# Optimization experiments

Hardware: AMD Instinct MI355X
Metric: run time of the kernel (lower is better)

The kernel has to match this reference:

```python
import jax, jax.numpy as jnp
import numpy as np

L, C = 32, 32          # latent_length, latent_classes
REC = 2048             # recurrent_size
PRIOR_COEF, POST_COEF, FREE_NAT = 0.8, 0.2, 1.0


def _kl(logits_p, logits_q):
    p = jax.nn.softmax(logits_p, axis=-1)
    log_p = jax.nn.log_softmax(logits_p, axis=-1)
    log_q = jax.nn.log_softmax(logits_q, axis=-1)
    return (p * (log_p - log_q)).sum(axis=(-2, -1))


def setup_inputs() -> dict:
    key = jax.random.key(0)
    ks = jax.random.split(key, 16)
    B, T = 256, 64
    s = 0.02  # weight scale to keep activations sane
    return {
        "zs": jax.random.normal(ks[0], (B, T, 4, 16, 32), jnp.float32),
        "actions": jax.random.normal(ks[1], (B, T, 3), jnp.float32),
        "z_mean": jnp.zeros((4, 1, 1), jnp.float32),
        "z_std": jnp.ones((4, 1, 1), jnp.float32),
        "enc_W": jax.random.normal(ks[2], (2048, 1024), jnp.float32) * s,
        "enc_b": jnp.zeros((1024,), jnp.float32),
        "pre_W": jax.random.normal(ks[3], (1027, 1024), jnp.float32) * s,
        "pre_b": jnp.zeros((1024,), jnp.float32),
        "W_ih": jax.random.normal(ks[4], (3 * REC, 1024), jnp.float32) * s,
        "W_hh": jax.random.normal(ks[5], (3 * REC, REC), jnp.float32) * s,
        "b_ih": jnp.zeros((3 * REC,), jnp.float32),
        "b_hh": jnp.zeros((3 * REC,), jnp.float32),
        "tW1": jax.random.normal(ks[6], (REC, 1024), jnp.float32) * s,
        "tb1": jnp.zeros((1024,), jnp.float32),
        "tW2": jax.random.normal(ks[7], (1024, L * C), jnp.float32) * s,
        "tb2": jnp.zeros((L * C,), jnp.float32),
        "rW1": jax.random.normal(ks[8], (REC + 1024, 1024), jnp.float32) * s,
        "rb1": jnp.zeros((1024,), jnp.float32),
        "rW2": jax.random.normal(ks[9], (1024, L * C), jnp.float32) * s,
        "rb2": jnp.zeros((L * C,), jnp.float32),
        "dW1": jax.random.normal(ks[10], (REC + L * C, 1024), jnp.float32) * s,
        "db1": jnp.zeros((1024,), jnp.float32),
        "dW2": jax.random.normal(ks[11], (1024, 2048), jnp.float32) * s,
        "db2": jnp.zeros((2048,), jnp.float32),
    }


def reference(zs, actions, z_mean, z_std, enc_W, enc_b, pre_W, pre_b,
              W_ih, W_hh, b_ih, b_hh, tW1, tb1, tW2, tb2,
              rW1, rb1, rW2, rb2, dW1, db1, dW2, db2):
    B, T = zs.shape[:2]
    zs_norm = (zs - z_mean) / z_std                      # (B,T,4,16,32)
    flat = zs_norm.reshape(B, T, -1)                      # (B,T,2048)
    encoded = jax.nn.elu(flat @ enc_W + enc_b)            # (B,T,1024)

    h0 = jnp.zeros((B, REC), zs.dtype)
    lat0 = jnp.zeros((B, L * C), zs.dtype)

    def step(carry, xs):
        h, lat = carry
        a_prev, emb = xs                                  # (B,3), (B,1024)
        # recurrent model: pre-MLP + GRU cell (PyTorch GRUCell math)
        x = jax.nn.elu(jnp.concatenate([lat, a_prev], -1) @ pre_W + pre_b)
        gx = x @ W_ih.T + b_ih                            # (B,3*REC)
        gh = h @ W_hh.T + b_hh
        xr, xz, xn = jnp.split(gx, 3, axis=-1)
        hr, hz, hn = jnp.split(gh, 3, axis=-1)
        r = jax.nn.sigmoid(xr + hr)
        u = jax.nn.sigmoid(xz + hz)
        n = jnp.tanh(xn + r * hn)
        h_new = (1.0 - u) * n + u * h
        # transition (prior) logits
        prior = (jax.nn.elu(h_new @ tW1 + tb1) @ tW2 + tb2).reshape(B, L, C)
        # representation (posterior) logits + straight-through one-hot sample
        post = (jax.nn.elu(jnp.concatenate([h_new, emb], -1) @ rW1 + rb1)
                @ rW2 + rb2).reshape(B, L, C)
        probs = jax.nn.softmax(post, axis=-1)
        one_hot = jax.nn.one_hot(jnp.argmax(post, -1), C, dtype=post.dtype)
        lat_new = (one_hot + probs - jax.lax.stop_gradient(probs)).reshape(B, L * C)
        return (h_new, lat_new), (h_new, lat_new, prior, post)

    xs = (jnp.swapaxes(actions[:, :-1], 0, 1),            # (T-1,B,3)
          jnp.swapaxes(encoded[:, 1:], 0, 1))             # (T-1,B,1024)
    _, (hiddens, latents, priors, posts) = jax.lax.scan(step, (h0, lat0), xs)
    hiddens = jnp.swapaxes(hiddens, 0, 1)                 # (B,T-1,REC)
    latents = jnp.swapaxes(latents, 0, 1)                 # (B,T-1,L*C)
    priors = jnp.swapaxes(priors, 0, 1)                   # (B,T-1,L,C)
    posts = jnp.swapaxes(posts, 0, 1)

    dec_in = jnp.concatenate([hiddens, latents], -1)
    pred = (jax.nn.elu(dec_in @ dW1 + db1) @ dW2 + db2).reshape(B, T - 1, 4, 16, 32)

    recon = jnp.mean((pred - zs_norm[:, 1:]) ** 2)
    prior_loss = PRIOR_COEF * jnp.maximum(
        _kl(jax.lax.stop_gradient(posts), priors), FREE_NAT)
    post_loss = POST_COEF * jnp.maximum(
        _kl(posts, jax.lax.stop_gradient(priors)), FREE_NAT)
    kl_loss = jnp.mean(prior_loss + post_loss)
    return recon + kl_loss
```

## Files before the change

kernel.cpp:

```cpp
#include <hip/hip_runtime.h>
#include <hip/hip_bf16.h>
#include <math.h>

typedef unsigned short u16;
typedef __attribute__((ext_vector_type(8))) short s16x8;
typedef __attribute__((ext_vector_type(4))) short s16x4;
typedef __attribute__((ext_vector_type(4))) float f32x4;

#define DEVI static __device__ __forceinline__

DEVI u16 f2bfu(float f) {
    unsigned u = __float_as_uint(f);
    unsigned r = (u + 0x7fffu + ((u >> 16) & 1u)) >> 16;
    return (u16)r;
}
DEVI float bfu2f(u16 u) { return __uint_as_float(((unsigned)u) << 16); }
DEVI float eluf(float x) { return x > 0.f ? x : (expf(x) - 1.f); }
DEVI float sigm(float x) { return 1.f / (1.f + expf(-x)); }

#define GLOAD16(gsrc, ldst)                                                            \
    __builtin_amdgcn_global_load_lds(                                                  \
        (__attribute__((address_space(1))) void*)(void*)(gsrc),                        \
        (__attribute__((address_space(3))) void*)(ldst), 16, 0, 0)

template <int N> DEVI void vmwait();
template <> DEVI void vmwait<0>() { asm volatile("s_waitcnt vmcnt(0)" ::: "memory"); }
template <> DEVI void vmwait<4>() { asm volatile("s_waitcnt vmcnt(4)" ::: "memory"); }
template <> DEVI void vmwait<5>() { asm volatile("s_waitcnt vmcnt(5)" ::: "memory"); }

struct GP {
    const u16* A; int lda;
    const u16* Bt;
    float* Cf; u16* Cb; int ldc;
    const float* bias;
    const u16* aux; int auxld;
    const float* zs;
    const float* zmean; const float* zstd;
    double* accum;
    int* idx;
    int K; int gridN; int rbase;
};

template <int MF, int NF, int EPI, bool DUAL>
__global__ __launch_bounds__(256) void gemm_k(GP p0, GP p1) {
    GP p = (DUAL && blockIdx.y) ? p1 : p0;
    constexpr int BM = 32 * MF, BN = 32 * NF;
    constexpr int ABYTES = BM * 64, BBYTES = BN * 64;

    const int tid = threadIdx.x;
    const int w = tid >> 6, lane = tid & 63;
    const int bid = blockIdx.x;
    const int bn = bid % p.gridN, bm = bid / p.gridN;
    const int r0 = bm * BM, c0 = bn * BN;
    const int wm = w >> 1, wn = w & 1;

    __shared__ __attribute__((aligned(16))) char sm[2 * (ABYTES + BBYTES)];
    __shared__ float ps[4];

    auto stage = [&](int kt, int buf) {
        char* s = sm + buf * (ABYTES + BBYTES);
        const u16* Ag = p.A + (size_t)r0 * p.lda + kt * 32;
#pragma unroll
        for (int it = 0; it < BM / 64; ++it) {
            int bo = it * 4096 + w * 1024 + lane * 16;
            int row = bo >> 6, kg = (bo & 63) >> 4;
            GLOAD16(Ag + (size_t)row * p.lda + kg * 8, s + bo);
        }
        const u16* Bg = p.Bt + (size_t)c0 * p.K + kt * 32;
        char* sb = s + ABYTES;
#pragma unroll
        for (int it = 0; it < BN / 64; ++it) {
            int bo = it * 4096 + w * 1024 + lane * 16;
            int row = bo >> 6, kg = (bo & 63) >> 4;
            GLOAD16(Bg + (size_t)row * p.K + kg * 8, sb + bo);
        }
    };

    f32x4 acc[MF][NF];
#pragma unroll
    for (int mf = 0; mf < MF; ++mf)
#pragma unroll
        for (int nf = 0; nf < NF; ++nf) acc[mf][nf] = (f32x4){0.f, 0.f, 0.f, 0.f};

    const int nk = p.K >> 5;
    stage(0, 0);
    asm volatile("s_waitcnt vmcnt(0)" ::: "memory");
    __syncthreads();
    int cur = 0;
    for (int kt = 0; kt < nk; ++kt) {
        if (kt + 1 < nk) stage(kt + 1, cur ^ 1);
        const char* s = sm + cur * (ABYTES + BBYTES);
        s16x8 aF[MF], bF[NF];
#pragma unroll
        for (int mf = 0; mf < MF; ++mf)
            aF[mf] = *(const s16x8*)(s + ((wm * MF + mf) * 16 + (lane & 15)) * 64 + (lane >> 4) * 16);
#pragma unroll
        for (int nf = 0; nf < NF; ++nf)
            bF[nf] = *(const s16x8*)(s + ABYTES + ((wn * NF + nf) * 16 + (lane & 15)) * 64 + (lane >> 4) * 16);
#pragma unroll
        for (int mf = 0; mf < MF; ++mf)
#pragma unroll
            for (int nf = 0; nf < NF; ++nf)
                acc[mf][nf] = __builtin_amdgcn_mfma_f32_16x16x32_bf16(aF[mf], bF[nf], acc[mf][nf], 0, 0, 0);
        asm volatile("s_waitcnt vmcnt(0)" ::: "memory");
        __syncthreads();
        cur ^= 1;
    }

    const int lrow4 = (lane >> 4) << 2, lcol = lane & 15;
    float lsum = 0.f;
#pragma unroll
    for (int mf = 0; mf < MF; ++mf) {
        int rowb = r0 + (wm * MF + mf) * 16 + lrow4;
#pragma unroll
        for (int nf = 0; nf < NF; ++nf) {
            int col = c0 + (wn * NF + nf) * 16 + lcol;
#pragma unroll
            for (int j = 0; j < 4; ++j) {
                float v = acc[mf][nf][j];
                int r = rowb + j;
                if constexpr (EPI == 1) {
                    p.Cb[(size_t)r * p.ldc + col] = f2bfu(eluf(v + p.bias[col]));
                } else if constexpr (EPI == 2) {
                    p.Cb[(size_t)r * p.ldc + col] = f2bfu(v + p.bias[col]);
                } else if constexpr (EPI == 4) {
                    p.Cb[(size_t)r * p.ldc + col] = f2bfu(eluf(v + bfu2f(p.aux[(size_t)r * p.auxld + col])));
                } else if constexpr (EPI == 5) {
                    v += p.bias[col];
                    int R = r + p.rbase;
                    int tt = R >> 8, b = R & 255;
                    int ch = col >> 9;
                    float z = (p.zs[((size_t)b * 64 + tt + 1) * 2048 + col] - p.zmean[ch]) / p.zstd[ch];
                    float d = v - z;
                    lsum += d * d;
                }
            }
        }
    }
    if constexpr (EPI == 5) {
#pragma unroll
        for (int o = 32; o > 0; o >>= 1) lsum += __shfl_down(lsum, o, 64);
        if (lane == 0) ps[w] = lsum;
        __syncthreads();
        if (tid == 0) {
            double s = (double)ps[0] + (double)ps[1] + (double)ps[2] + (double)ps[3];
            atomicAdd(p.accum, s);
        }
    }
}

template <int EPI, int MF, int NF>
DEVI void epiS(const GP& p, f32x4 (&acc)[MF][NF], int r0, int c0, int wm, int wn,
               int lrow4, int lcol) {
#pragma unroll
    for (int mf = 0; mf < MF; ++mf) {
        int rowb = r0 + (wm * MF + mf) * 16 + lrow4;
#pragma unroll
        for (int nf = 0; nf < NF; ++nf) {
            int col = c0 + (wn * NF + nf) * 16 + lcol;
#pragma unroll
            for (int j = 0; j < 4; ++j) {
                float v = acc[mf][nf][j];
                int r = rowb + j;
                if constexpr (EPI == 4) {
                    p.Cb[(size_t)r * p.ldc + col] = f2bfu(eluf(v + bfu2f(p.aux[(size_t)r * p.auxld + col])));
                } else if constexpr (EPI == 7) {
                    p.Cb[(size_t)r * p.ldc + col] = f2bfu(v + p.bias[col]);
                }
            }
        }
    }
}

template <int WM, int WN, int MF, int NF, int EPIa, int EPIb>
__global__ __launch_bounds__(WM * WN * 64) void gemmS(GP pa, GP pb, int nA) {
    constexpr int NT = WM * WN * 64;
    constexpr int BM = WM * MF * 16, BN = WN * NF * 16;
    constexpr int ABY = BM * 128, BBY = BN * 128;
    constexpr int LPT = (ABY + BBY) / (NT * 16);

    const int tid = threadIdx.x, w = tid >> 6, lane = tid & 63;
    const bool isA = (int)blockIdx.x < nA;
    GP p = isA ? pa : pb;
    const int bid = isA ? blockIdx.x : blockIdx.x - nA;
    const int bn = bid % p.gridN, bm = bid / p.gridN;
    const int r0 = bm * BM, c0 = bn * BN;
    const int wm = w / WN, wn = w % WN;

    __shared__ __attribute__((aligned(16))) char sm[3 * (ABY + BBY)];

    auto stage = [&](int kt, int buf) {
        char* s = sm + buf * (ABY + BBY);
#pragma unroll
        for (int it = 0; it < ABY / (NT * 16); ++it) {
            int bo = it * (NT * 16) + tid * 16;
            int row = bo >> 7, kb = bo & 127;
            int kbs = kb ^ ((row & 7) << 4);
            GLOAD16(p.A + (size_t)(r0 + row) * p.lda + kt * 64 + (kbs >> 1), s + bo);
        }
        char* sb = s + ABY;
#pragma unroll
        for (int it = 0; it < BBY / (NT * 16); ++it) {
            int bo = it * (NT * 16) + tid * 16;
            int row = bo >> 7, kb = bo & 127;
            int kbs = kb ^ ((row & 7) << 4);
            GLOAD16(p.Bt + (size_t)(c0 + row) * p.K + kt * 64 + (kbs >> 1), sb + bo);
        }
    };

    f32x4 acc[MF][NF];
#pragma unroll
    for (int mf = 0; mf < MF; ++mf)
#pragma unroll
        for (int nf = 0; nf < NF; ++nf) acc[mf][nf] = (f32x4){0.f, 0.f, 0.f, 0.f};

    const int nk = p.K >> 6;
    stage(0, 0);
    stage(1, 1);
    int b0 = 0, b1 = 1, b2 = 2;
    for (int kt = 0; kt < nk; ++kt) {
        if (kt < nk - 1) vmwait<LPT>(); else vmwait<0>();
        __builtin_amdgcn_sched_barrier(0);
        __builtin_amdgcn_s_barrier();
        if (kt + 2 < nk) stage(kt + 2, b2);
        const char* s = sm + b0 * (ABY + BBY);
#pragma unroll
        for (int ks = 0; ks < 2; ++ks) {
            const int kb = ks * 64 + ((lane >> 4) << 4);
            s16x8 aF[MF], bF[NF];
#pragma unroll
            for (int mf = 0; mf < MF; ++mf) {
                int rt = (wm * MF + mf) * 16 + (lane & 15);
                aF[mf] = *(const s16x8*)(s + rt * 128 + (kb ^ ((rt & 7) << 4)));
            }
#pragma unroll
            for (int nf = 0; nf < NF; ++nf) {
                int rt = (wn * NF + nf) * 16 + (lane & 15);
                bF[nf] = *(const s16x8*)(s + ABY + rt * 128 + (kb ^ ((rt & 7) << 4)));
            }
#pragma unroll
            for (int mf = 0; mf < MF; ++mf)
#pragma unroll
                for (int nf = 0; nf < NF; ++nf)
                    acc[mf][nf] = __builtin_amdgcn_mfma_f32_16x16x32_bf16(aF[mf], bF[nf], acc[mf][nf], 0, 0, 0);
        }
        int t_ = b0; b0 = b1; b1 = b2; b2 = t_;
    }

    const int lrow4 = (lane >> 4) << 2, lcol = lane & 15;
    if constexpr (EPIa == 8) {
        const int lat = (c0 >> 5) + wn;
#pragma unroll
        for (int mf = 0; mf < MF; ++mf) {
#pragma unroll
            for (int j = 0; j < 4; ++j) {
                int r = r0 + (wm * MF + mf) * 16 + lrow4 + j;
                int col0 = c0 + wn * 32 + lcol;
                float v0 = acc[mf][0][j] + p.bias[col0];
                float v1 = acc[mf][1][j] + p.bias[col0 + 16];
                p.Cb[(size_t)r * p.ldc + col0] = f2bfu(v0);
                p.Cb[(size_t)r * p.ldc + col0 + 16] = f2bfu(v1);
                float mv; int mi;
                if (v1 > v0) { mv = v1; mi = lcol + 16; } else { mv = v0; mi = lcol; }
#pragma unroll
                for (int o = 8; o >= 1; o >>= 1) {
                    float ov = __shfl_xor(mv, o, 64);
                    int oi = __shfl_xor(mi, o, 64);
                    if (ov > mv || (ov == mv && oi < mi)) { mv = ov; mi = oi; }
                }
                if (lcol == 0) p.idx[(size_t)r * 32 + lat] = mi;
            }
        }
    } else {
        if (isA) epiS<EPIa, MF, NF>(p, acc, r0, c0, wm, wn, lrow4, lcol);
        else     epiS<EPIb, MF, NF>(p, acc, r0, c0, wm, wn, lrow4, lcol);
    }
}

template <bool FIRST>
__global__ __launch_bounds__(256) void k_gates(const u16* __restrict__ X, const u16* __restrict__ WihB,
                                               const float* __restrict__ bih, const float* __restrict__ bhh,
                                               const u16* __restrict__ GHb, float* __restrict__ hf32,
                                               u16* __restrict__ hallT) {
    constexpr int ABY = 64 * 128;
    constexpr int BTB = 32 * 128;
    constexpr int TSZ = ABY + 3 * BTB;
    const int tid = threadIdx.x, w = tid >> 6, lane = tid & 63;
    const int bm = blockIdx.x >> 6, bn = blockIdx.x & 63;
    const int r0 = bm * 64, c0 = bn * 32;
    const int wm = w >> 1, wn = w & 1;

    __shared__ __attribute__((aligned(16))) char sm[3 * TSZ];

    auto stage = [&](int kt, int buf) {
        char* s = sm + buf * TSZ;
#pragma unroll
        for (int it = 0; it < 2; ++it) {
            int bo = it * 4096 + tid * 16;
            int row = bo >> 7, kb = bo & 127;
            int kbs = kb ^ ((row & 7) << 4);
            GLOAD16(X + (size_t)(r0 + row) * 1024 + kt * 64 + (kbs >> 1), s + bo);
        }
        char* sb = s + ABY;
#pragma unroll
        for (int g = 0; g < 3; ++g) {
            int bo = tid * 16;
            int row = bo >> 7, kb = bo & 127;
            int kbs = kb ^ ((row & 7) << 4);
            GLOAD16(WihB + (size_t)(g * 2048 + c0 + row) * 1024 + kt * 64 + (kbs >> 1), sb + g * BTB + bo);
        }
    };

    f32x4 acc[3][2];
#pragma unroll
    for (int g = 0; g < 3; ++g)
#pragma unroll
        for (int mf = 0; mf < 2; ++mf) acc[g][mf] = (f32x4){0.f, 0.f, 0.f, 0.f};

    stage(0, 0);
    stage(1, 1);
    int b0 = 0, b1 = 1, b2 = 2;
    for (int kt = 0; kt < 16; ++kt) {
        if (kt < 15) vmwait<5>(); else vmwait<0>();
        __builtin_amdgcn_sched_barrier(0);
        __builtin_amdgcn_s_barrier();
        if (kt + 2 < 16) stage(kt + 2, b2);
        const char* s = sm + b0 * TSZ;
#pragma unroll
        for (int ks = 0; ks < 2; ++ks) {
            const int kb = ks * 64 + ((lane >> 4) << 4);
            s16x8 aF[2], bF[3];
#pragma unroll
            for (int mf = 0; mf < 2; ++mf) {
                int rt = (wm * 2 + mf) * 16 + (lane & 15);
                aF[mf] = *(const s16x8*)(s + rt * 128 + (kb ^ ((rt & 7) << 4)));
            }
#pragma unroll
            for (int g = 0; g < 3; ++g) {
                int rt = wn * 16 + (lane & 15);
                bF[g] = *(const s16x8*)(s + ABY + g * BTB + rt * 128 + (kb ^ ((rt & 7) << 4)));
            }
#pragma unroll
            for (int g = 0; g < 3; ++g)
#pragma unroll
                for (int mf = 0; mf < 2; ++mf)
                    acc[g][mf] = __builtin_amdgcn_mfma_f32_16x16x32_bf16(aF[mf], bF[g], acc[g][mf], 0, 0, 0);
        }
        int t_ = b0; b0 = b1; b1 = b2; b2 = t_;
    }

    const int lrow4 = (lane >> 4) << 2, lcol = lane & 15;
    const int cc = c0 + wn * 16 + lcol;
#pragma unroll
    for (int mf = 0; mf < 2; ++mf) {
        int rr0 = r0 + (wm * 2 + mf) * 16 + lrow4;
#pragma unroll
        for (int j = 0; j < 4; ++j) {
            int rr = rr0 + j;
            float xr = acc[0][mf][j] + bih[cc];
            float xz = acc[1][mf][j] + bih[2048 + cc];
            float xn = acc[2][mf][j] + bih[4096 + cc];
            float hr_, hz_, hn_;
            if (FIRST) { hr_ = bhh[cc]; hz_ = bhh[2048 + cc]; hn_ = bhh[4096 + cc]; }
            else {
                const u16* g = GHb + (size_t)rr * 6144;
                hr_ = bfu2f(g[cc]); hz_ = bfu2f(g[2048 + cc]); hn_ = bfu2f(g[4096 + cc]);
            }
            float r = sigm(xr + hr_);
            float u = sigm(xz + hz_);
            float n = tanhf(xn + r * hn_);
            float hold = FIRST ? 0.f : hf32[(size_t)rr * 2048 + cc];
            float h = (1.f - u) * n + u * hold;
            hf32[(size_t)rr * 2048 + cc] = h;
            hallT[(size_t)rr * 2048 + cc] = f2bfu(h);
        }
    }
}

__global__ void k_init(double* acc) { acc[0] = 0.0; acc[1] = 0.0; }

__global__ void k_cast(const float* __restrict__ src, u16* __restrict__ dst, int n4) {
    int i = blockIdx.x * 256 + threadIdx.x;
    if (i >= n4) return;
    f32x4 v = *(const f32x4*)(src + (size_t)i * 4);
    s16x4 o;
    o[0] = (short)f2bfu(v[0]); o[1] = (short)f2bfu(v[1]);
    o[2] = (short)f2bfu(v[2]); o[3] = (short)f2bfu(v[3]);
    *(s16x4*)(dst + (size_t)i * 4) = o;
}

__global__ void k_transpose(const float* __restrict__ src, int sld, u16* __restrict__ dst, int K) {
    __shared__ float tile[32][33];
    int k0 = blockIdx.x * 32, n0 = blockIdx.y * 32;
    for (int r = threadIdx.y; r < 32; r += 8)
        tile[r][threadIdx.x] = src[(size_t)(k0 + r) * sld + n0 + threadIdx.x];
    __syncthreads();
    for (int r = threadIdx.y; r < 32; r += 8)
        dst[(size_t)(n0 + r) * K + k0 + threadIdx.x] = f2bfu(tile[threadIdx.x][r]);
}

__global__ void k_prep(const float* __restrict__ zsp, const float* __restrict__ zm,
                       const float* __restrict__ zsd, u16* __restrict__ flat) {
    size_t i = ((size_t)blockIdx.x * 256 + threadIdx.x) * 4;
    f32x4 v = *(const f32x4*)(zsp + i);
    int ch = ((int)(i >> 9)) & 3;
    float m = zm[ch], s = zsd[ch];
    s16x4 o;
    o[0] = (short)f2bfu((v[0] - m) / s); o[1] = (short)f2bfu((v[1] - m) / s);
    o[2] = (short)f2bfu((v[2] - m) / s); o[3] = (short)f2bfu((v[3] - m) / s);
    *(s16x4*)(flat + i) = o;
}

__global__ __launch_bounds__(256) void k_xpre0(const float* __restrict__ preW, const float* __restrict__ preb,
                                               const float* __restrict__ actions, u16* __restrict__ xout) {
    int b = blockIdx.x, tid = threadIdx.x;
    __shared__ float as[3];
    if (tid < 3) as[tid] = actions[(size_t)b * 64 * 3 + tid];
    __syncthreads();
    for (int j = tid; j < 1024; j += 256) {
        float s = preb[j] + as[0] * preW[1024 * 1024 + j] + as[1] * preW[1025 * 1024 + j] + as[2] * preW[1026 * 1024 + j];
        xout[(b << 10) + j] = f2bfu(eluf(s));
    }
}

__global__ __launch_bounds__(256) void k_xgen(const int* __restrict__ latidx_t,
                                              const u16* __restrict__ PreLatB, const float* __restrict__ preW,
                                              const float* __restrict__ preb,
                                              const float* __restrict__ actions, u16* __restrict__ xout,
                                              int tnext) {
    int b = blockIdx.x, tid = threadIdx.x;
    __shared__ int idxs[32];
    __shared__ float as[3];
    if (tid < 32) idxs[tid] = latidx_t[(b << 5) + tid];
    if (tid >= 64 && tid < 67) as[tid - 64] = actions[((size_t)b * 64 + tnext) * 3 + (tid - 64)];
    __syncthreads();
    const int j4 = tid * 4;
    f32x4 s = *(const f32x4*)(preb + j4);
#pragma unroll
    for (int cc = 0; cc < 3; ++cc) {
        f32x4 wv = *(const f32x4*)(preW + (size_t)(1024 + cc) * 1024 + j4);
        s[0] += as[cc] * wv[0]; s[1] += as[cc] * wv[1];
        s[2] += as[cc] * wv[2]; s[3] += as[cc] * wv[3];
    }
#pragma unroll
    for (int l = 0; l < 32; ++l) {
        s16x4 v = *(const s16x4*)(PreLatB + (size_t)((l << 5) + idxs[l]) * 1024 + j4);
        s[0] += bfu2f((u16)v[0]); s[1] += bfu2f((u16)v[1]);
        s[2] += bfu2f((u16)v[2]); s[3] += bfu2f((u16)v[3]);
    }
    s16x4 o;
    o[0] = (short)f2bfu(eluf(s[0])); o[1] = (short)f2bfu(eluf(s[1]));
    o[2] = (short)f2bfu(eluf(s[2])); o[3] = (short)f2bfu(eluf(s[3]));
    *(s16x4*)(xout + (b << 10) + j4) = o;
}

__global__ __launch_bounds__(256) void k_kl(const u16* __restrict__ PoAll, const u16* __restrict__ PrAll,
                                            float* __restrict__ klrow) {
    int m = blockIdx.x, tid = threadIdx.x;
    const u16* Po = PoAll + (size_t)m * 1024;
    const u16* Pr = PrAll + (size_t)m * 1024;
    __shared__ float klpart[32];
    int grp = tid >> 5, c = tid & 31;
#pragma unroll
    for (int it = 0; it < 4; ++it) {
        int l = it * 8 + grp;
        float po = bfu2f(Po[l * 32 + c]);
        float pr = bfu2f(Pr[l * 32 + c]);
        float mv = po, mq = pr;
#pragma unroll
        for (int o = 16; o > 0; o >>= 1) {
            mv = fmaxf(mv, __shfl_xor(mv, o, 32));
            mq = fmaxf(mq, __shfl_xor(mq, o, 32));
        }
        float ep = expf(po - mv), eq = expf(pr - mq);
        float sp = ep, sq = eq;
#pragma unroll
        for (int o = 16; o > 0; o >>= 1) { sp += __shfl_xor(sp, o, 32); sq += __shfl_xor(sq, o, 32); }
        float logp = po - mv - logf(sp);
        float logq = pr - mq - logf(sq);
        float klc = (ep / sp) * (logp - logq);
#pragma unroll
        for (int o = 16; o > 0; o >>= 1) klc += __shfl_xor(klc, o, 32);
        if (c == 0) klpart[l] = klc;
    }
    __syncthreads();
    if (tid == 0) {
        float kl = 0.f;
        for (int l = 0; l < 32; ++l) kl += klpart[l];
        klrow[m] = fmaxf(kl, 1.0f);
    }
}

__global__ __launch_bounds__(256) void k_latsum(const u16* __restrict__ LatB, const float* __restrict__ db1,
                                                const int* __restrict__ latidx_all, u16* __restrict__ latsum) {
    int m = blockIdx.x, tid = threadIdx.x;
    __shared__ int idxs[32];
    if (tid < 32) idxs[tid] = latidx_all[(size_t)m * 32 + tid];
    __syncthreads();
    const int j4 = tid * 4;
    f32x4 s = *(const f32x4*)(db1 + j4);
#pragma unroll
    for (int l = 0; l < 32; ++l) {
        s16x4 v = *(const s16x4*)(LatB + (size_t)((l << 5) + idxs[l]) * 1024 + j4);
        s[0] += bfu2f((u16)v[0]); s[1] += bfu2f((u16)v[1]);
        s[2] += bfu2f((u16)v[2]); s[3] += bfu2f((u16)v[3]);
    }
    s16x4 o;
    o[0] = (short)f2bfu(s[0]); o[1] = (short)f2bfu(s[1]);
    o[2] = (short)f2bfu(s[2]); o[3] = (short)f2bfu(s[3]);
    *(s16x4*)(latsum + (size_t)m * 1024 + j4) = o;
}

__global__ __launch_bounds__(256) void k_finalize(const double* __restrict__ acc,
                                                  const float* __restrict__ klrow, float* __restrict__ out) {
    __shared__ double ps[256];
    int tid = threadIdx.x;
    double s = 0.0;
    for (int i = tid; i < 16128; i += 256) s += (double)klrow[i];
    ps[tid] = s;
    __syncthreads();
    for (int o = 128; o > 0; o >>= 1) {
        if (tid < o) ps[tid] += ps[tid + o];
        __syncthreads();
    }
    if (tid == 0) out[0] = (float)(acc[0] / 33030144.0 + ps[0] / 16128.0);
}

extern "C" void kernel_launch(void* const* d_in, const int* in_sizes, int n_in,
                              void* d_out, int out_size, void* d_ws, size_t ws_size,
                              hipStream_t stream) {
    const float* zs      = (const float*)d_in[0];
    const float* actions = (const float*)d_in[1];
    const float* zmean   = (const float*)d_in[2];
    const float* zstd    = (const float*)d_in[3];
    const float* encW    = (const float*)d_in[4];
    const float* encb    = (const float*)d_in[5];
    const float* preW    = (const float*)d_in[6];
    const float* preb    = (const float*)d_in[7];
    const float* Wih     = (const float*)d_in[8];
    const float* Whh     = (const float*)d_in[9];
    const float* bih     = (const float*)d_in[10];
    const float* bhh     = (const float*)d_in[11];
    const float* tW1     = (const float*)d_in[12];
    const float* tb1     = (const float*)d_in[13];
    const float* tW2     = (const float*)d_in[14];
    const float* tb2     = (const float*)d_in[15];
    const float* rW1     = (const float*)d_in[16];
    const float* rb1     = (const float*)d_in[17];
    const float* rW2     = (const float*)d_in[18];
    const float* rb2     = (const float*)d_in[19];
    const float* dW1     = (const float*)d_in[20];
    const float* db1     = (const float*)d_in[21];
    const float* dW2     = (const float*)d_in[22];
    const float* db2     = (const float*)d_in[23];

    char* W = (char*)d_ws;
    size_t off = 0;
    auto take = [&](size_t b) { char* p = W + off; off += (b + 255) & ~(size_t)255; return p; };

    double* accum  = (double*)take(16);
    u16* encWbt = (u16*)take((size_t)1024 * 2048 * 2);
    u16* WihB   = (u16*)take((size_t)6144 * 1024 * 2);
    u16* WhhB   = (u16*)take((size_t)6144 * 2048 * 2);
    u16* l1B    = (u16*)take((size_t)2048 * 2048 * 2);
    u16* tW2bt  = (u16*)take((size_t)1024 * 1024 * 2);
    u16* rW2bt  = (u16*)take((size_t)1024 * 1024 * 2);
    u16* rW1bbt = (u16*)take((size_t)1024 * 1024 * 2);
    u16* dW1abt = (u16*)take((size_t)1024 * 2048 * 2);
    u16* dW2bt  = (u16*)take((size_t)2048 * 1024 * 2);
    u16* PreLatB = (u16*)take((size_t)1024 * 1024 * 2);
    u16* LatB    = (u16*)take((size_t)1024 * 1024 * 2);
    u16* Hall   = (u16*)take((size_t)63 * 256 * 2048 * 2);
    int* latidx = (int*)take((size_t)63 * 256 * 32 * 4);
    u16* embR   = (u16*)take((size_t)16384 * 1024 * 2);
    u16* enc    = (u16*)take((size_t)16384 * 1024 * 2);
    float* klrow = (float*)take((size_t)16128 * 4);
    u16* GHb    = (u16*)take((size_t)2 * 256 * 6144 * 2);
    float* hf32 = (float*)take((size_t)256 * 2048 * 4);
    u16* x_bf   = (u16*)take((size_t)256 * 1024 * 2);
    u16* p1q1   = (u16*)take((size_t)256 * 1024 * 2);
    char* X     = take((size_t)17825792);

    u16* flatc = (u16*)X;
    u16* Xp    = (u16*)X;
    u16* d1    = (u16*)X;
    u16* PoAll = enc;
    u16* PrAll = embR;

    k_init<<<1, 1, 0, stream>>>(accum);

    k_cast<<<6144, 256, 0, stream>>>(Wih, WihB, 6291456 / 4);
    k_cast<<<12288, 256, 0, stream>>>(Whh, WhhB, 12582912 / 4);
    k_cast<<<1024, 256, 0, stream>>>(preW, PreLatB, 262144);
    k_cast<<<1024, 256, 0, stream>>>(dW1 + (size_t)2048 * 1024, LatB, 262144);
    k_transpose<<<dim3(64, 32), dim3(32, 8), 0, stream>>>(encW, 1024, encWbt, 2048);
    k_transpose<<<dim3(64, 32), dim3(32, 8), 0, stream>>>(tW1, 1024, l1B, 2048);
    k_transpose<<<dim3(64, 32), dim3(32, 8), 0, stream>>>(rW1, 1024, l1B + (size_t)1024 * 2048, 2048);
    k_transpose<<<dim3(32, 32), dim3(32, 8), 0, stream>>>(tW2, 1024, tW2bt, 1024);
    k_transpose<<<dim3(32, 32), dim3(32, 8), 0, stream>>>(rW2, 1024, rW2bt, 1024);
    k_transpose<<<dim3(32, 32), dim3(32, 8), 0, stream>>>(rW1 + (size_t)2048 * 1024, 1024, rW1bbt, 1024);
    k_transpose<<<dim3(64, 32), dim3(32, 8), 0, stream>>>(dW1, 1024, dW1abt, 2048);
    k_transpose<<<dim3(32, 64), dim3(32, 8), 0, stream>>>(dW2, 2048, dW2bt, 1024);

    for (int pass = 0; pass < 4; ++pass) {
        k_prep<<<8192, 256, 0, stream>>>(zs + (size_t)pass * 4096 * 2048, zmean, zstd, flatc);
        GP e{}; e.A = flatc; e.lda = 2048; e.Bt = encWbt; e.Cb = enc + (size_t)pass * 4096 * 1024;
        e.ldc = 1024; e.bias = encb; e.K = 2048; e.gridN = 8;
        gemm_k<4, 4, 1, false><<<dim3(256), 256, 0, stream>>>(e, e);
    }
    {
        GP e{}; e.A = enc; e.lda = 1024; e.Bt = rW1bbt; e.Cb = embR; e.ldc = 1024;
        e.bias = rb1; e.K = 1024; e.gridN = 8;
        gemm_k<4, 4, 2, false><<<dim3(1024), 256, 0, stream>>>(e, e);
    }

    k_xpre0<<<256, 256, 0, stream>>>(preW, preb, actions, x_bf);
    for (int t = 0; t < 63; ++t) {
        if (t == 0)
            k_gates<true><<<256, 256, 0, stream>>>(x_bf, WihB, bih, bhh, GHb, hf32, Hall);
        else
            k_gates<false><<<256, 256, 0, stream>>>(x_bf, WihB, bih, bhh, GHb + (size_t)(t & 1) * 256 * 6144,
                                                    hf32, Hall + (size_t)t * 256 * 2048);
        {
            GP pa{}; pa.A = Hall + (size_t)t * 256 * 2048; pa.lda = 2048; pa.Bt = WhhB;
            pa.Cb = GHb + (size_t)((t + 1) & 1) * 256 * 6144; pa.ldc = 6144; pa.bias = bhh;
            pa.K = 2048; pa.gridN = 96;
            GP pb{}; pb.A = Hall + (size_t)t * 256 * 2048; pb.lda = 2048;
            pb.Bt = l1B + (size_t)1024 * 2048; pb.Cb = p1q1; pb.ldc = 1024;
            pb.aux = embR + (size_t)(t + 1) * 1024; pb.auxld = 65536;
            pb.K = 2048; pb.gridN = 16;
            int nA = (t < 62) ? 384 : 0;
            gemmS<2, 2, 2, 2, 7, 4><<<dim3(nA + 64), 256, 0, stream>>>(pa, pb, nA);
        }
        {
            GP q{}; q.A = p1q1; q.lda = 1024; q.Bt = rW2bt; q.ldc = 1024;
            q.Cb = PoAll + (size_t)t * 256 * 1024; q.bias = rb2; q.K = 1024; q.gridN = 16;
            q.idx = latidx + (size_t)t * 256 * 32;
            gemmS<2, 2, 2, 2, 8, 8><<<dim3(64), 256, 0, stream>>>(q, q, 64);
        }
        if (t < 62)
            k_xgen<<<256, 256, 0, stream>>>(latidx + (size_t)t * 256 * 32,
                                            PreLatB, preW, preb, actions, x_bf, t + 1);
    }

    for (int half = 0; half < 2; ++half) {
        int m0 = half * 8064;
        GP e{}; e.A = Hall + (size_t)m0 * 2048; e.lda = 2048; e.Bt = l1B; e.Cb = Xp; e.ldc = 1024;
        e.bias = tb1; e.K = 2048; e.gridN = 8;
        gemm_k<4, 4, 1, false><<<dim3(504), 256, 0, stream>>>(e, e);
        GP q{}; q.A = Xp; q.lda = 1024; q.Bt = tW2bt; q.Cb = PrAll + (size_t)m0 * 1024; q.ldc = 1024;
        q.bias = tb2; q.K = 1024; q.gridN = 8;
        gemm_k<4, 4, 2, false><<<dim3(504), 256, 0, stream>>>(q, q);
    }
    k_kl<<<16128, 256, 0, stream>>>(PoAll, PrAll, klrow);

    k_latsum<<<16128, 256, 0, stream>>>(LatB, db1, latidx, embR);
    for (int half = 0; half < 2; ++half) {
        int m0 = half * 8064;
        GP d{}; d.A = Hall + (size_t)m0 * 2048; d.lda = 2048; d.Bt = dW1abt; d.Cb = d1; d.ldc = 1024;
        d.aux = embR + (size_t)m0 * 1024; d.auxld = 1024; d.K = 2048; d.gridN = 8;
        gemm_k<4, 4, 4, false><<<dim3(504), 256, 0, stream>>>(d, d);
        GP d2{}; d2.A = d1; d2.lda = 1024; d2.Bt = dW2bt; d2.ldc = 2048; d2.bias = db2;
        d2.zs = zs; d2.zmean = zmean; d2.zstd = zstd; d2.accum = accum; d2.K = 1024; d2.gridN = 16;
        d2.rbase = m0;
        gemm_k<4, 4, 5, false><<<dim3(1008), 256, 0, stream>>>(d2, d2);
    }
    k_finalize<<<1, 256, 0, stream>>>(accum, klrow, (float*)d_out);
}
```

Measured before the change: 3.623 ms.

## Replace double-buffered gemm_k with triple-buffered gemmS and retune per-step tiles

Removes the older double-buffered gemm_k kernel and routes all bulk GEMMs (encoder, embedding, prior, decoder, recon loss) through the gemmS template, which uses a 3-stage LDS pipeline with K-step 64. The recon-loss epilogue (EPI 5) moves into gemmS. Tile shapes change to 128x64 for bulk GEMMs, giving more blocks. Inside the recurrent loop, the W_hh/posterior GEMM uses wider N tiles (fewer blocks) and the posterior-head GEMM uses smaller M tiles (more blocks). This trades wait-for-all double buffering for deeper prefetch, and changes per-step occupancy.

```diff
diff --git a/kernel.cpp b/kernel.cpp
--- a/kernel.cpp
+++ b/kernel.cpp
@@ -25,8 +25,10 @@
 
 template <int N> DEVI void vmwait();
 template <> DEVI void vmwait<0>() { asm volatile("s_waitcnt vmcnt(0)" ::: "memory"); }
+template <> DEVI void vmwait<3>() { asm volatile("s_waitcnt vmcnt(3)" ::: "memory"); }
 template <> DEVI void vmwait<4>() { asm volatile("s_waitcnt vmcnt(4)" ::: "memory"); }
 template <> DEVI void vmwait<5>() { asm volatile("s_waitcnt vmcnt(5)" ::: "memory"); }
+template <> DEVI void vmwait<6>() { asm volatile("s_waitcnt vmcnt(6)" ::: "memory"); }
 
 struct GP {
     const u16* A; int lda;
@@ -41,74 +43,9 @@
     int K; int gridN; int rbase;
 };
 
-template <int MF, int NF, int EPI, bool DUAL>
-__global__ __launch_bounds__(256) void gemm_k(GP p0, GP p1) {
-    GP p = (DUAL && blockIdx.y) ? p1 : p0;
-    constexpr int BM = 32 * MF, BN = 32 * NF;
-    constexpr int ABYTES = BM * 64, BBYTES = BN * 64;
-
-    const int tid = threadIdx.x;
-    const int w = tid >> 6, lane = tid & 63;
-    const int bid = blockIdx.x;
-    const int bn = bid % p.gridN, bm = bid / p.gridN;
-    const int r0 = bm * BM, c0 = bn * BN;
-    const int wm = w >> 1, wn = w & 1;
-
-    __shared__ __attribute__((aligned(16))) char sm[2 * (ABYTES + BBYTES)];
-    __shared__ float ps[4];
-
-    auto stage = [&](int kt, int buf) {
-        char* s = sm + buf * (ABYTES + BBYTES);
-        const u16* Ag = p.A + (size_t)r0 * p.lda + kt * 32;
-#pragma unroll
-        for (int it = 0; it < BM / 64; ++it) {
-            int bo = it * 4096 + w * 1024 + lane * 16;
-            int row = bo >> 6, kg = (bo & 63) >> 4;
-            GLOAD16(Ag + (size_t)row * p.lda + kg * 8, s + bo);
-        }
-        const u16* Bg = p.Bt + (size_t)c0 * p.K + kt * 32;
-        char* sb = s + ABYTES;
-#pragma unroll
-        for (int it = 0; it < BN / 64; ++it) {
-            int bo = it * 4096 + w * 1024 + lane * 16;
-            int row = bo >> 6, kg = (bo & 63) >> 4;
-            GLOAD16(Bg + (size_t)row * p.K + kg * 8, sb + bo);
-        }
-    };
-
-    f32x4 acc[MF][NF];
-#pragma unroll
-    for (int mf = 0; mf < MF; ++mf)
-#pragma unroll
-        for (int nf = 0; nf < NF; ++nf) acc[mf][nf] = (f32x4){0.f, 0.f, 0.f, 0.f};
-
-    const int nk = p.K >> 5;
-    stage(0, 0);
-    asm volatile("s_waitcnt vmcnt(0)" ::: "memory");
-    __syncthreads();
-    int cur = 0;
-    for (int kt = 0; kt < nk; ++kt) {
-        if (kt + 1 < nk) stage(kt + 1, cur ^ 1);
-        const char* s = sm + cur * (ABYTES + BBYTES);
-        s16x8 aF[MF], bF[NF];
-#pragma unroll
-        for (int mf = 0; mf < MF; ++mf)
-            aF[mf] = *(const s16x8*)(s + ((wm * MF + mf) * 16 + (lane & 15)) * 64 + (lane >> 4) * 16);
-#pragma unroll
-        for (int nf = 0; nf < NF; ++nf)
-            bF[nf] = *(const s16x8*)(s + ABYTES + ((wn * NF + nf) * 16 + (lane & 15)) * 64 + (lane >> 4) * 16);
-#pragma unroll
-        for (int mf = 0; mf < MF; ++mf)
-#pragma unroll
-            for (int nf = 0; nf < NF; ++nf)
-                acc[mf][nf] = __builtin_amdgcn_mfma_f32_16x16x32_bf16(aF[mf], bF[nf], acc[mf][nf], 0, 0, 0);
-        asm volatile("s_waitcnt vmcnt(0)" ::: "memory");
-        __syncthreads();
-        cur ^= 1;
-    }
-
-    const int lrow4 = (lane >> 4) << 2, lcol = lane & 15;
-    float lsum = 0.f;
+template <int EPI, int MF, int NF>
+DEVI void epiS(const GP& p, f32x4 (&acc)[MF][NF], int r0, int c0, int wm, int wn,
+               int lrow4, int lcol) {
 #pragma unroll
     for (int mf = 0; mf < MF; ++mf) {
         int rowb = r0 + (wm * MF + mf) * 16 + lrow4;
@@ -125,45 +62,6 @@
                     p.Cb[(size_t)r * p.ldc + col] = f2bfu(v + p.bias[col]);
                 } else if constexpr (EPI == 4) {
                     p.Cb[(size_t)r * p.ldc + col] = f2bfu(eluf(v + bfu2f(p.aux[(size_t)r * p.auxld + col])));
-                } else if constexpr (EPI == 5) {
-                    v += p.bias[col];
-                    int R = r + p.rbase;
-                    int tt = R >> 8, b = R & 255;
-                    int ch = col >> 9;
-                    float z = (p.zs[((size_t)b * 64 + tt + 1) * 2048 + col] - p.zmean[ch]) / p.zstd[ch];
-                    float d = v - z;
-                    lsum += d * d;
-                }
-            }
-        }
-    }
-    if constexpr (EPI == 5) {
-#pragma unroll
-        for (int o = 32; o > 0; o >>= 1) lsum += __shfl_down(lsum, o, 64);
-        if (lane == 0) ps[w] = lsum;
-        __syncthreads();
-        if (tid == 0) {
-            double s = (double)ps[0] + (double)ps[1] + (double)ps[2] + (double)ps[3];
-            atomicAdd(p.accum, s);
-        }
-    }
-}
-
-template <int EPI, int MF, int NF>
-DEVI void epiS(const GP& p, f32x4 (&acc)[MF][NF], int r0, int c0, int wm, int wn,
-               int lrow4, int lcol) {
-#pragma unroll
-    for (int mf = 0; mf < MF; ++mf) {
-        int rowb = r0 + (wm * MF + mf) * 16 + lrow4;
-#pragma unroll
-        for (int nf = 0; nf < NF; ++nf) {
-            int col = c0 + (wn * NF + nf) * 16 + lcol;
-#pragma unroll
-            for (int j = 0; j < 4; ++j) {
-                float v = acc[mf][nf][j];
-                int r = rowb + j;
-                if constexpr (EPI == 4) {
-                    p.Cb[(size_t)r * p.ldc + col] = f2bfu(eluf(v + bfu2f(p.aux[(size_t)r * p.auxld + col])));
                 } else if constexpr (EPI == 7) {
                     p.Cb[(size_t)r * p.ldc + col] = f2bfu(v + p.bias[col]);
                 }
@@ -188,6 +86,7 @@
     const int wm = w / WN, wn = w % WN;
 
     __shared__ __attribute__((aligned(16))) char sm[3 * (ABY + BBY)];
+    __shared__ float ps_[WM * WN];
 
     auto stage = [&](int kt, int buf) {
         char* s = sm + buf * (ABY + BBY);
@@ -270,6 +169,36 @@
                 }
                 if (lcol == 0) p.idx[(size_t)r * 32 + lat] = mi;
             }
+        }
+    } else if constexpr (EPIa == 5) {
+        float lsum = 0.f;
+#pragma unroll
+        for (int mf = 0; mf < MF; ++mf) {
+            int rowb = r0 + (wm * MF + mf) * 16 + lrow4;
+#pragma unroll
+            for (int nf = 0; nf < NF; ++nf) {
+                int col = c0 + (wn * NF + nf) * 16 + lcol;
+#pragma unroll
+                for (int j = 0; j < 4; ++j) {
+                    float v = acc[mf][nf][j] + p.bias[col];
+                    int R = rowb + j + p.rbase;
+                    int tt = R >> 8, b = R & 255;
+                    int ch = col >> 9;
+                    float z = (p.zs[((size_t)b * 64 + tt + 1) * 2048 + col] - p.zmean[ch]) / p.zstd[ch];
+                    float d = v - z;
+                    lsum += d * d;
+                }
+            }
+        }
+#pragma unroll
+        for (int o = 32; o > 0; o >>= 1) lsum += __shfl_down(lsum, o, 64);
+        if (lane == 0) ps_[w] = lsum;
+        __syncthreads();
+        if (tid == 0) {
+            double s = 0.0;
+#pragma unroll
+            for (int i = 0; i < WM * WN; ++i) s += (double)ps_[i];
+            atomicAdd(p.accum, s);
         }
     } else {
         if (isA) epiS<EPIa, MF, NF>(p, acc, r0, c0, wm, wn, lrow4, lcol);
@@ -605,13 +534,13 @@
     for (int pass = 0; pass < 4; ++pass) {
         k_prep<<<8192, 256, 0, stream>>>(zs + (size_t)pass * 4096 * 2048, zmean, zstd, flatc);
         GP e{}; e.A = flatc; e.lda = 2048; e.Bt = encWbt; e.Cb = enc + (size_t)pass * 4096 * 1024;
-        e.ldc = 1024; e.bias = encb; e.K = 2048; e.gridN = 8;
-        gemm_k<4, 4, 1, false><<<dim3(256), 256, 0, stream>>>(e, e);
+        e.ldc = 1024; e.bias = encb; e.K = 2048; e.gridN = 16;
+        gemmS<2, 2, 4, 2, 1, 1><<<dim3(512), 256, 0, stream>>>(e, e, 512);
     }
     {
         GP e{}; e.A = enc; e.lda = 1024; e.Bt = rW1bbt; e.Cb = embR; e.ldc = 1024;
-        e.bias = rb1; e.K = 1024; e.gridN = 8;
-        gemm_k<4, 4, 2, false><<<dim3(1024), 256, 0, stream>>>(e, e);
+        e.bias = rb1; e.K = 1024; e.gridN = 16;
+        gemmS<2, 2, 4, 2, 2, 2><<<dim3(2048), 256, 0, stream>>>(e, e, 2048);
     }
 
     k_xpre0<<<256, 256, 0, stream>>>(preW, preb, actions, x_bf);
@@ -624,19 +553,19 @@
         {
             GP pa{}; pa.A = Hall + (size_t)t * 256 * 2048; pa.lda = 2048; pa.Bt = WhhB;
             pa.Cb = GHb + (size_t)((t + 1) & 1) * 256 * 6144; pa.ldc = 6144; pa.bias = bhh;
-            pa.K = 2048; pa.gridN = 96;
+            pa.K = 2048; pa.gridN = 48;
             GP pb{}; pb.A = Hall + (size_t)t * 256 * 2048; pb.lda = 2048;
             pb.Bt = l1B + (size_t)1024 * 2048; pb.Cb = p1q1; pb.ldc = 1024;
             pb.aux = embR + (size_t)(t + 1) * 1024; pb.auxld = 65536;
-            pb.K = 2048; pb.gridN = 16;
-            int nA = (t < 62) ? 384 : 0;
-            gemmS<2, 2, 2, 2, 7, 4><<<dim3(nA + 64), 256, 0, stream>>>(pa, pb, nA);
+            pb.K = 2048; pb.gridN = 8;
+            int nA = (t < 62) ? 192 : 0;
+            gemmS<2, 2, 2, 4, 7, 4><<<dim3(nA + 32), 256, 0, stream>>>(pa, pb, nA);
         }
         {
             GP q{}; q.A = p1q1; q.lda = 1024; q.Bt = rW2bt; q.ldc = 1024;
             q.Cb = PoAll + (size_t)t * 256 * 1024; q.bias = rb2; q.K = 1024; q.gridN = 16;
             q.idx = latidx + (size_t)t * 256 * 32;
-            gemmS<2, 2, 2, 2, 8, 8><<<dim3(64), 256, 0, stream>>>(q, q, 64);
+            gemmS<2, 2, 1, 2, 8, 8><<<dim3(128), 256, 0, stream>>>(q, q, 128);
         }
         if (t < 62)
             k_xgen<<<256, 256, 0, stream>>>(latidx + (size_t)t * 256 * 32,
@@ -646,11 +575,11 @@
     for (int half = 0; half < 2; ++half) {
         int m0 = half * 8064;
         GP e{}; e.A = Hall + (size_t)m0 * 2048; e.lda = 2048; e.Bt = l1B; e.Cb = Xp; e.ldc = 1024;
-        e.bias = tb1; e.K = 2048; e.gridN = 8;
-        gemm_k<4, 4, 1, false><<<dim3(504), 256, 0, stream>>>(e, e);
+        e.bias = tb1; e.K = 2048; e.gridN = 16;
+        gemmS<2, 2, 4, 2, 1, 1><<<dim3(1008), 256, 0, stream>>>(e, e, 1008);
         GP q{}; q.A = Xp; q.lda = 1024; q.Bt = tW2bt; q.Cb = PrAll + (size_t)m0 * 1024; q.ldc = 1024;
-        q.bias = tb2; q.K = 1024; q.gridN = 8;
-        gemm_k<4, 4, 2, false><<<dim3(504), 256, 0, stream>>>(q, q);
+        q.bias = tb2; q.K = 1024; q.gridN = 16;
+        gemmS<2, 2, 4, 2, 2, 2><<<dim3(1008), 256, 0, stream>>>(q, q, 1008);
     }
     k_kl<<<16128, 256, 0, stream>>>(PoAll, PrAll, klrow);
 
@@ -658,12 +587,12 @@
     for (int half = 0; half < 2; ++half) {
         int m0 = half * 8064;
         GP d{}; d.A = Hall + (size_t)m0 * 2048; d.lda = 2048; d.Bt = dW1abt; d.Cb = d1; d.ldc = 1024;
-        d.aux = embR + (size_t)m0 * 1024; d.auxld = 1024; d.K = 2048; d.gridN = 8;
-        gemm_k<4, 4, 4, false><<<dim3(504), 256, 0, stream>>>(d, d);
+        d.aux = embR + (size_t)m0 * 1024; d.auxld = 1024; d.K = 2048; d.gridN = 16;
+        gemmS<2, 2, 4, 2, 4, 4><<<dim3(1008), 256, 0, stream>>>(d, d, 1008);
         GP d2{}; d2.A = d1; d2.lda = 1024; d2.Bt = dW2bt; d2.ldc = 2048; d2.bias = db2;
-        d2.zs = zs; d2.zmean = zmean; d2.zstd = zstd; d2.accum = accum; d2.K = 1024; d2.gridN = 16;
+        d2.zs = zs; d2.zmean = zmean; d2.zstd = zstd; d2.accum = accum; d2.K = 1024; d2.gridN = 32;
         d2.rbase = m0;
-        gemm_k<4, 4, 5, false><<<dim3(1008), 256, 0, stream>>>(d2, d2);
+        gemmS<2, 2, 4, 2, 5, 5><<<dim3(2016), 256, 0, stream>>>(d2, d2, 2016);
     }
     k_finalize<<<1, 256, 0, stream>>>(accum, klrow, (float*)d_out);
 }
```

Measured after the change: 3.738 ms. 3.2% more time.
